# Kernel optimization log

Hardware: AMD Instinct MI355X
Metric: run time of the kernel (lower is better)

## Reference

```python
import jax, jax.numpy as jnp
import numpy as np


def _unfold(x, ks, pad):
    # torch nn.Unfold ordering: flattened channel dim is (c, kh, kw), output (b, c*ks*ks, h*w)
    b, c, h, w = x.shape
    if ks == 1:
        return x.reshape(b, c, h * w)
    xp = jnp.pad(x, ((0, 0), (0, 0), (pad, pad), (pad, pad)))
    patches = jnp.stack([xp[:, :, i:i + h, j:j + w] for i in range(ks) for j in range(ks)], axis=2)  # (b,c,ks*ks,h,w)
    return patches.reshape(b, c * ks * ks, h * w)


def _cg_conv(x, weight, ce_w, gd_w, gd2_w, ci_w, ks, pad, g=8):
    # Content-gated conv: SE-style dynamic kernel generation + unfold + batched matmul
    b, c, h, w = x.shape
    oc = weight.shape[0]
    # AdaptiveMaxPool2d((ks,ks)); h,w divisible by ks so bins are uniform
    gl = x.reshape(b, c, ks, h // ks, ks, w // ks).max(axis=(3, 5)).reshape(b, c, ks * ks)
    ce2 = jnp.einsum('bck,nk->bcn', gl, ce_w)                      # (b,c,num_lat)
    out = jnp.einsum('bcn,kn->bck', jax.nn.relu(ce2), gd_w)        # (b,c,ks*ks)
    # channel path: (b,c//g,g,num_lat) -> transpose -> Linear(g -> oc/(c//g))
    t = jax.nn.relu(jnp.transpose(ce2.reshape(b, c // g, g, -1), (0, 1, 3, 2)))
    ocp = jnp.transpose(jnp.einsum('bpng,og->bpno', t, ci_w), (0, 1, 3, 2)).reshape(b, oc, -1)
    ocp = jnp.einsum('bon,kn->bok', jax.nn.relu(ocp), gd2_w)       # (b,oc,ks*ks)
    dyn = jax.nn.sigmoid(out[:, None, :, :] + ocp[:, :, None, :])  # (b,oc,c,ks*ks)
    dyn = dyn * weight.reshape(1, oc, c, ks * ks)
    x_un = _unfold(x, ks, pad)                                     # (b, c*ks*ks, h*w)
    y = jnp.einsum('bok,bkl->bol', dyn.reshape(b, oc, c * ks * ks), x_un)
    return y.reshape(b, oc, h, w)


def setup_inputs() -> dict:
    key = jax.random.key(0)
    ks_ = jax.random.split(key, 12)
    b, c_in, c_hid, c_out, H, W = 4, 64, 256, 64, 96, 96
    s = 0.02
    inp = {
        'x': jax.random.normal(ks_[0], (b, c_in, H, W), jnp.float32),
        # fc1: 1x1, num_lat = 1, ci: 8 -> 256//(64//8)=32
        'fc1_weight': jax.random.normal(ks_[1], (c_hid, c_in, 1, 1), jnp.float32) * s,
        'fc1_ce': jax.random.normal(ks_[2], (1, 1), jnp.float32) * s,
        'fc1_gd': jax.random.normal(ks_[3], (1, 1), jnp.float32) * s,
        'fc1_gd2': jax.random.normal(ks_[4], (1, 1), jnp.float32) * s,
        'fc1_ci': jax.random.normal(ks_[5], (32, 8), jnp.float32) * s,
        # fc2: 3x3, num_lat = 5, ci: 8 -> 64//(256//8)=2
        'fc2_weight': jax.random.normal(ks_[6], (c_out, c_hid, 3, 3), jnp.float32) * s,
        'fc2_ce': jax.random.normal(ks_[7], (5, 9), jnp.float32) * s,
        'fc2_gd': jax.random.normal(ks_[8], (9, 5), jnp.float32) * s,
        'fc2_gd2': jax.random.normal(ks_[9], (9, 5), jnp.float32) * s,
        'fc2_ci': jax.random.normal(ks_[10], (2, 8), jnp.float32) * s,
    }
    return inp


def reference(x, fc1_weight, fc1_ce, fc1_gd, fc1_gd2, fc1_ci,
              fc2_weight, fc2_ce, fc2_gd, fc2_gd2, fc2_ci):
    h = _cg_conv(x, fc1_weight, fc1_ce, fc1_gd, fc1_gd2, fc1_ci, ks=1, pad=0)
    h = jax.nn.gelu(h, approximate=False)  # torch nn.GELU default is exact erf
    return _cg_conv(h, fc2_weight, fc2_ce, fc2_gd, fc2_gd2, fc2_ci, ks=3, pad=1)
```

## Files before the change

kernel.cpp:

```cpp
#include <hip/hip_runtime.h>
#include <math.h>

typedef __attribute__((ext_vector_type(8))) short short8x;
typedef __attribute__((ext_vector_type(4))) float float4x;
typedef unsigned short u16;
typedef unsigned int u32;

__device__ __forceinline__ float bf2f(u16 u) {
    return __uint_as_float(((u32)u) << 16);
}
__device__ __forceinline__ u16 f2bf(float f) {
    u32 u = __float_as_uint(f);
    u32 r = (u + 0x7fffu + ((u >> 16) & 1u)) >> 16;
    return (u16)r;
}
__device__ __forceinline__ u32 fenc(float f) {
    u32 b = __float_as_uint(f);
    return b ^ (0x80000000u | (u32)((int)b >> 31));
}
__device__ __forceinline__ float fdec(u32 u) {
    u32 b = (u & 0x80000000u) ? (u ^ 0x80000000u) : ~u;
    return __uint_as_float(b);
}
__device__ __forceinline__ float fsig(float v) {
    return __builtin_amdgcn_rcpf(1.f + __expf(-v));
}
__device__ __forceinline__ float fgelu(float v) {
    const float is2 = 0.70710678118654752f;
    float z = v * is2;
    float ax = fabsf(z);
    float t = __builtin_amdgcn_rcpf(1.f + 0.3275911f * ax);
    float p = ((((1.061405429f * t - 1.453152027f) * t) + 1.421413741f) * t - 0.284496736f) * t
              + 0.254829592f;
    float e = 1.f - p * t * __expf(-ax * ax);
    float er = copysignf(e, z);
    return 0.5f * v * (1.f + er);
}


__global__ __launch_bounds__(256) void k_gl1(const float* __restrict__ x, float* __restrict__ gl1,
                                             u32* __restrict__ h2p32, u32* __restrict__ gl2u) {
    if (blockIdx.x >= 256) {
        int t = threadIdx.x;
        int plane_id = blockIdx.x - 256;
        u32* plane = h2p32 + plane_id * (98 * 98 * 16);
        for (int i = t; i < 1568; i += 256) plane[i] = 0u;
        for (int i = t; i < 1568; i += 256) plane[97 * 98 * 16 + i] = 0u;
        for (int i = t; i < 3072; i += 256) {
            int r = (i >> 5) + 1;
            int p = ((i >> 4) & 1) * 97;
            int w = i & 15;
            plane[(r * 98 + p) * 16 + w] = 0u;
        }
        for (int i = plane_id * 288 + t; i < (plane_id + 1) * 288; i += 256)
            gl2u[i] = 0u;
        return;
    }
    int b = blockIdx.x >> 6, c = blockIdx.x & 63;
    const float4* p = (const float4*)(x + (b * 64 + c) * 9216);
    float m = -1e30f;
    #pragma unroll
    for (int i = 0; i < 9; i++) {
        float4 v = p[i * 256 + threadIdx.x];
        m = fmaxf(m, fmaxf(fmaxf(v.x, v.y), fmaxf(v.z, v.w)));
    }
    __shared__ float red[256];
    red[threadIdx.x] = m;
    __syncthreads();
    for (int s = 128; s > 0; s >>= 1) {
        if (threadIdx.x < s) red[threadIdx.x] = fmaxf(red[threadIdx.x], red[threadIdx.x + s]);
        __syncthreads();
    }
    if (threadIdx.x == 0) gl1[b * 64 + c] = red[0];
}

__global__ __launch_bounds__(256) void k_gate1(const float* __restrict__ gl1,
                                               const float* __restrict__ ce, const float* __restrict__ gd,
                                               const float* __restrict__ gd2, const float* __restrict__ ci,
                                               const float* __restrict__ w1, u16* __restrict__ W1A) {
    int b = blockIdx.x >> 4, s = blockIdx.x & 15;
    int t = threadIdx.x;
    __shared__ float rce[64], out1[64], ocp[256];
    float cew = ce[0], gdw = gd[0], gd2w = gd2[0];
    if (t < 64) {
        float r = fmaxf(gl1[b * 64 + t] * cew, 0.f);
        rce[t] = r;
        out1[t] = r * gdw;
    }
    __syncthreads();
    {
        int p = t >> 5, oi = t & 31;
        float sv = 0.f;
        #pragma unroll
        for (int g = 0; g < 8; g++) sv += rce[p * 8 + g] * ci[oi * 8 + g];
        ocp[t] = fmaxf(sv, 0.f) * gd2w;
    }
    __syncthreads();
    u16* Wb = W1A + b * 256 * 64;
    #pragma unroll
    for (int i = 0; i < 4; i++) {
        int idx = s * 1024 + i * 256 + t;
        int o = idx >> 6, c = idx & 63;
        float v = out1[c] + ocp[o];
        Wb[idx] = f2bf(fsig(v) * w1[idx]);
    }
}

__global__ __launch_bounds__(256) void k_gemm1(const u16* __restrict__ W1A, const float* __restrict__ x,
                                               u16* __restrict__ h2p, u32* __restrict__ gl2u) {
    int bi = blockIdx.x;
    int b = bi / 192, rem = bi % 192;
    int y = rem >> 1, half = rem & 1;
    int t = threadIdx.x, wave = t >> 6, lane = t & 63, l15 = lane & 15, quad = lane >> 4;

    __shared__ __align__(16) u16 xs[48 * 72];
    const float* xb = x + (b * 64) * 9216 + y * 96 + half * 48;
    const float2* xb2 = (const float2*)xb;
    #pragma unroll
    for (int i = 0; i < 6; i++) {
        int idx = i * 256 + t;
        int c = idx / 24, px2 = idx - c * 24;
        float2 v = xb2[c * 4608 + px2];
        int px = px2 * 2;
        xs[px * 72 + c] = f2bf(v.x);
        xs[(px + 1) * 72 + c] = f2bf(v.y);
    }
    __syncthreads();

    float4x acc[4][3];
    #pragma unroll
    for (int mt = 0; mt < 4; mt++)
        #pragma unroll
        for (int nt = 0; nt < 3; nt++) acc[mt][nt] = (float4x){0.f, 0.f, 0.f, 0.f};
    const u16* Wb = W1A + b * 256 * 64;
    #pragma unroll
    for (int c0 = 0; c0 < 64; c0 += 32) {
        short8x bfr[3];
        #pragma unroll
        for (int nt = 0; nt < 3; nt++)
            bfr[nt] = *(const short8x*)(xs + (nt * 16 + l15) * 72 + c0 + quad * 8);
        #pragma unroll
        for (int mt = 0; mt < 4; mt++) {
            int oc = wave * 64 + mt * 16 + l15;
            short8x afr = *(const short8x*)(Wb + oc * 64 + c0 + quad * 8);
            #pragma unroll
            for (int nt = 0; nt < 3; nt++)
                acc[mt][nt] = __builtin_amdgcn_mfma_f32_16x16x32_bf16(afr, bfr[nt], acc[mt][nt], 0, 0, 0);
        }
    }
    float gf[4][3][4];
    #pragma unroll
    for (int mt = 0; mt < 4; mt++) {
        #pragma unroll
        for (int nt = 0; nt < 3; nt++) {
            int xx = half * 48 + nt * 16 + l15;
            int oc0 = wave * 64 + mt * 16 + quad * 4;
            int g = oc0 >> 5, cl = oc0 & 31;
            u16 pk[4];
            #pragma unroll
            for (int r = 0; r < 4; r++) {
                float gl = fgelu(acc[mt][nt][r]);
                gf[mt][nt][r] = gl;
                pk[r] = f2bf(gl);
            }
            u16* dst = h2p + ((((b * 8 + g) * 98 + y + 1) * 98) + xx + 1) * 32 + cl;
            *(ushort4*)dst = make_ushort4(pk[0], pk[1], pk[2], pk[3]);
        }
    }
    int ki = y >> 5;
    int kA = ki * 3 + (half == 0 ? 0 : 1);
    int kB = ki * 3 + (half == 0 ? 1 : 2);
    #pragma unroll
    for (int mt = 0; mt < 4; mt++) {
        float vA[4], vB[4];
        #pragma unroll
        for (int r = 0; r < 4; r++) {
            if (half == 0) { vA[r] = fmaxf(gf[mt][0][r], gf[mt][1][r]); vB[r] = gf[mt][2][r]; }
            else           { vA[r] = gf[mt][0][r]; vB[r] = fmaxf(gf[mt][1][r], gf[mt][2][r]); }
        }
        #pragma unroll
        for (int m = 1; m < 16; m <<= 1) {
            #pragma unroll
            for (int r = 0; r < 4; r++) {
                vA[r] = fmaxf(vA[r], __shfl_xor(vA[r], m));
                vB[r] = fmaxf(vB[r], __shfl_xor(vB[r], m));
            }
        }
        if (l15 == 0) {
            #pragma unroll
            for (int r = 0; r < 4; r++) {
                int oc = wave * 64 + mt * 16 + quad * 4 + r;
                atomicMax(&gl2u[(b * 9 + kA) * 256 + oc], fenc(vA[r]));
                atomicMax(&gl2u[(b * 9 + kB) * 256 + oc], fenc(vB[r]));
            }
        }
    }
}

__global__ __launch_bounds__(256) void k_gate2(const u32* __restrict__ gl2u,
                                               const float* __restrict__ ce, const float* __restrict__ gd,
                                               const float* __restrict__ gd2, const float* __restrict__ ci,
                                               const float* __restrict__ w2, u16* __restrict__ W2A) {
    int b = blockIdx.x >> 4, s = blockIdx.x & 15;
    int t = threadIdx.x;
    __shared__ float rce[256][5];
    __shared__ float out2[256][9];
    __shared__ float ocp2[64][9];
    {
        float gl[9];
        #pragma unroll
        for (int k = 0; k < 9; k++) gl[k] = fdec(gl2u[(b * 9 + k) * 256 + t]);
        float r[5];
        #pragma unroll
        for (int n = 0; n < 5; n++) {
            float sv = 0.f;
            #pragma unroll
            for (int k = 0; k < 9; k++) sv += gl[k] * ce[n * 9 + k];
            r[n] = fmaxf(sv, 0.f);
            rce[t][n] = r[n];
        }
        #pragma unroll
        for (int k = 0; k < 9; k++) {
            float sv = 0.f;
            #pragma unroll
            for (int n = 0; n < 5; n++) sv += r[n] * gd[k * 5 + n];
            out2[t][k] = sv;
        }
    }
    __syncthreads();
    if (t < 64) {
        int p = t >> 1, oi = t & 1;
        float rt[5];
        #pragma unroll
        for (int n = 0; n < 5; n++) {
            float sv = 0.f;
            #pragma unroll
            for (int g = 0; g < 8; g++) sv += rce[p * 8 + g][n] * ci[oi * 8 + g];
            rt[n] = fmaxf(sv, 0.f);
        }
        #pragma unroll
        for (int k = 0; k < 9; k++) {
            float sv = 0.f;
            #pragma unroll
            for (int n = 0; n < 5; n++) sv += rt[n] * gd2[k * 5 + n];
            ocp2[t][k] = sv;
        }
    }
    __syncthreads();
    u16* Wb = W2A + b * (8 * 9 * 64 * 32);
    for (int it = 0; it < 36; it++) {
        int flat = s * 9216 + it * 256 + t;
        int cl = flat & 31;
        int o = (flat >> 5) & 63;
        int rest = flat >> 11;
        int k = rest % 9, g = rest / 9;
        int c = g * 32 + cl;
        float v = out2[c][k] + ocp2[o][k];
        Wb[flat] = f2bf(fsig(v) * w2[(o * 256 + c) * 9 + k]);
    }
}

__global__ __launch_bounds__(256) void k_conv2(const u16* __restrict__ W2A, const u16* __restrict__ h2p,
                                               float* __restrict__ out) {
    int bi = blockIdx.x;
    int b = bi / 192, rem = bi % 192;
    int y = rem >> 1, half = rem & 1;
    int t = threadIdx.x, wave = t >> 6, lane = t & 63, l15 = lane & 15, quad = lane >> 4;
    __shared__ __align__(16) u16 Bls[2][3 * 50 * 32];

    int offs[3];
    #pragma unroll
    for (int j = 0; j < 3; j++) {
        int i = t + j * 256;
        int r = i / 200, c16 = i - r * 200;
        offs[j] = ((y + r) * 98 + half * 48) * 32 + c16 * 8;
    }
    const int plane_sz = 98 * 98 * 32;
    uint4 p0, p1, p2;
    {
        const u16* pl = h2p + (b * 8) * plane_sz;
        p0 = *(const uint4*)(pl + offs[0]);
        p1 = *(const uint4*)(pl + offs[1]);
        if (t < 88) p2 = *(const uint4*)(pl + offs[2]);
        uint4* Bd = (uint4*)Bls[0];
        Bd[t] = p0;
        Bd[t + 256] = p1;
        if (t < 88) Bd[t + 512] = p2;
    }

    float4x acc[3];
    #pragma unroll
    for (int nt = 0; nt < 3; nt++) acc[nt] = (float4x){0.f, 0.f, 0.f, 0.f};

    for (int g = 0; g < 8; g++) {
        __syncthreads();
        if (g < 7) {
            const u16* pl = h2p + (b * 8 + g + 1) * plane_sz;
            p0 = *(const uint4*)(pl + offs[0]);
            p1 = *(const uint4*)(pl + offs[1]);
            if (t < 88) p2 = *(const uint4*)(pl + offs[2]);
        }
        const u16* Wg = W2A + (b * 8 + g) * (9 * 64 * 32);
        const u16* Bcur = Bls[g & 1];
        #pragma unroll
        for (int k = 0; k < 9; k++) {
            int ki = k / 3, kj = k - ki * 3;
            short8x af = *(const short8x*)(Wg + (k * 64 + wave * 16 + l15) * 32 + quad * 8);
            #pragma unroll
            for (int nt = 0; nt < 3; nt++) {
                int pxl = nt * 16 + l15 + kj;
                short8x bf = *(const short8x*)(Bcur + (ki * 50 + pxl) * 32 + quad * 8);
                acc[nt] = __builtin_amdgcn_mfma_f32_16x16x32_bf16(af, bf, acc[nt], 0, 0, 0);
            }
        }
        if (g < 7) {
            uint4* Bd = (uint4*)Bls[(g + 1) & 1];
            Bd[t] = p0;
            Bd[t + 256] = p1;
            if (t < 88) Bd[t + 512] = p2;
        }
    }
    #pragma unroll
    for (int nt = 0; nt < 3; nt++) {
        int xx = half * 48 + nt * 16 + l15;
        #pragma unroll
        for (int r = 0; r < 4; r++) {
            int oc = wave * 16 + quad * 4 + r;
            out[((b * 64 + oc) * 96 + y) * 96 + xx] = acc[nt][r];
        }
    }
}

extern "C" void kernel_launch(void* const* d_in, const int* in_sizes, int n_in,
                              void* d_out, int out_size, void* d_ws, size_t ws_size,
                              hipStream_t stream) {
    const float* x    = (const float*)d_in[0];
    const float* w1   = (const float*)d_in[1];
    const float* ce1  = (const float*)d_in[2];
    const float* gd1  = (const float*)d_in[3];
    const float* gd21 = (const float*)d_in[4];
    const float* ci1  = (const float*)d_in[5];
    const float* w2   = (const float*)d_in[6];
    const float* ce2  = (const float*)d_in[7];
    const float* gd2  = (const float*)d_in[8];
    const float* gd22 = (const float*)d_in[9];
    const float* ci2  = (const float*)d_in[10];
    float* out = (float*)d_out;

    char* ws = (char*)d_ws;
    u16*   h2p  = (u16*)(ws + 4718592);
    u16*   W1A  = (u16*)(ws + 24387584);
    u16*   W2A  = (u16*)(ws + 24518656);
    float* gl1  = (float*)(ws + 25698304);
    u32*   gl2u = (u32*)(ws + 25796608);

    k_gl1  <<<288, 256, 0, stream>>>(x, gl1, (u32*)h2p, gl2u);
    k_gate1<<<64,  256, 0, stream>>>(gl1, ce1, gd1, gd21, ci1, w1, W1A);
    k_gemm1<<<768, 256, 0, stream>>>(W1A, x, h2p, gl2u);
    k_gate2<<<64,  256, 0, stream>>>(gl2u, ce2, gd2, gd22, ci2, w2, W2A);
    k_conv2<<<768, 256, 0, stream>>>(W2A, h2p, out);
}
```

Baseline: 131.8 us.

## Stage conv2 input tiles with direct global-to-LDS loads and swizzled layout

The conv2 kernel now fills its double-buffered LDS input tiles with global_load_lds 16-byte async copies instead of loading into registers and storing to LDS after the MFMA loop. The source addresses and the LDS read addresses get a matching XOR swizzle on the 16-byte column index to cut LDS bank conflicts on the MFMA B-fragment reads. A minimum-blocks hint is added to launch_bounds. This removes the staging registers and the explicit LDS store pass, but correctness depends on the barrier waiting for the async vmem-to-LDS writes to finish.

```diff
diff --git a/kernel.cpp b/kernel.cpp
--- a/kernel.cpp
+++ b/kernel.cpp
@@ -5,6 +5,12 @@
 typedef __attribute__((ext_vector_type(4))) float float4x;
 typedef unsigned short u16;
 typedef unsigned int u32;
+
+typedef const u32 __attribute__((address_space(1)))* gas_p;
+typedef u32 __attribute__((address_space(3)))* las_p;
+__device__ __forceinline__ void gl_lds16(const void* g, void* l) {
+    __builtin_amdgcn_global_load_lds((gas_p)g, (las_p)l, 16, 0, 0);
+}
 
 __device__ __forceinline__ float bf2f(u16 u) {
     return __uint_as_float(((u32)u) << 16);
@@ -260,8 +266,8 @@
     }
 }
 
-__global__ __launch_bounds__(256) void k_conv2(const u16* __restrict__ W2A, const u16* __restrict__ h2p,
-                                               float* __restrict__ out) {
+__global__ __launch_bounds__(256, 3) void k_conv2(const u16* __restrict__ W2A, const u16* __restrict__ h2p,
+                                                  float* __restrict__ out) {
     int bi = blockIdx.x;
     int b = bi / 192, rem = bi % 192;
     int y = rem >> 1, half = rem & 1;
@@ -272,20 +278,19 @@
     #pragma unroll
     for (int j = 0; j < 3; j++) {
         int i = t + j * 256;
-        int r = i / 200, c16 = i - r * 200;
+        int is = i ^ ((i >> 3) & 3);
+        int r = is / 200, c16 = is - r * 200;
         offs[j] = ((y + r) * 98 + half * 48) * 32 + c16 * 8;
     }
     const int plane_sz = 98 * 98 * 32;
-    uint4 p0, p1, p2;
+    int wb = wave * 512;
+
     {
         const u16* pl = h2p + (b * 8) * plane_sz;
-        p0 = *(const uint4*)(pl + offs[0]);
-        p1 = *(const uint4*)(pl + offs[1]);
-        if (t < 88) p2 = *(const uint4*)(pl + offs[2]);
-        uint4* Bd = (uint4*)Bls[0];
-        Bd[t] = p0;
-        Bd[t + 256] = p1;
-        if (t < 88) Bd[t + 512] = p2;
+        u16* d = &Bls[0][0];
+        gl_lds16(pl + offs[0], d + wb);
+        gl_lds16(pl + offs[1], d + 2048 + wb);
+        if (t < 88) gl_lds16(pl + offs[2], d + 4096 + wb);
     }
 
     float4x acc[3];
@@ -296,9 +301,10 @@
         __syncthreads();
         if (g < 7) {
             const u16* pl = h2p + (b * 8 + g + 1) * plane_sz;
-            p0 = *(const uint4*)(pl + offs[0]);
-            p1 = *(const uint4*)(pl + offs[1]);
-            if (t < 88) p2 = *(const uint4*)(pl + offs[2]);
+            u16* d = &Bls[(g + 1) & 1][0];
+            gl_lds16(pl + offs[0], d + wb);
+            gl_lds16(pl + offs[1], d + 2048 + wb);
+            if (t < 88) gl_lds16(pl + offs[2], d + 4096 + wb);
         }
         const u16* Wg = W2A + (b * 8 + g) * (9 * 64 * 32);
         const u16* Bcur = Bls[g & 1];
@@ -309,15 +315,11 @@
             #pragma unroll
             for (int nt = 0; nt < 3; nt++) {
                 int pxl = nt * 16 + l15 + kj;
-                short8x bf = *(const short8x*)(Bcur + (ki * 50 + pxl) * 32 + quad * 8);
+                int row = ki * 50 + pxl;
+                int qs = quad ^ ((row >> 1) & 3);
+                short8x bf = *(const short8x*)(Bcur + row * 32 + qs * 8);
                 acc[nt] = __builtin_amdgcn_mfma_f32_16x16x32_bf16(af, bf, acc[nt], 0, 0, 0);
             }
-        }
-        if (g < 7) {
-            uint4* Bd = (uint4*)Bls[(g + 1) & 1];
-            Bd[t] = p0;
-            Bd[t + 256] = p1;
-            if (t < 88) Bd[t + 512] = p2;
         }
     }
     #pragma unroll
```

Result: no change. 132.1 us (+0.2%).
